# Kernel tuning notes

Hardware: AMD Instinct MI355X
Metric: run time of the kernel (lower is better)

## Reference

```python
import jax, jax.numpy as jnp
import numpy as np

DIM = 512
HEADS = 8
DIM_HEAD = 64
INNER = HEADS * DIM_HEAD  # 512
TOPK_FRAC = 0.7
SCALE = DIM_HEAD ** -0.5


def setup_inputs() -> dict:
    key = jax.random.key(0)
    k1, k2, k3, k4 = jax.random.split(key, 4)
    B, N = 4, 1024
    x = jax.random.normal(k1, (B, N, DIM), dtype=jnp.float32)
    # nn.Linear(dim, inner*3, bias=False): weight [3*inner, dim]; store transposed for x @ W
    w_qkv = jax.random.normal(k2, (DIM, 3 * INNER), dtype=jnp.float32) * (DIM ** -0.5)
    # to_out Linear(inner, dim) with bias
    w_out = jax.random.normal(k3, (INNER, DIM), dtype=jnp.float32) * (INNER ** -0.5)
    b_out = jax.random.normal(k4, (DIM,), dtype=jnp.float32) * 0.01
    return {"x": x, "w_qkv": w_qkv, "w_out": w_out, "b_out": b_out}


def reference(x, w_qkv, w_out, b_out):
    B, N, _ = x.shape
    H, D = HEADS, DIM_HEAD
    qkv = x @ w_qkv  # [B, N, 3*INNER]
    q, k, v = jnp.split(qkv, 3, axis=-1)
    # 'b n (h d) -> b h n d'
    reshape = lambda t: t.reshape(B, N, H, D).transpose(0, 2, 1, 3)
    q, k, v = reshape(q), reshape(k), reshape(v)
    dots = jnp.einsum('bhid,bhjd->bhij', q, k) * SCALE  # [B, H, N, N]
    # per-row top-k masking (kNN attention)
    kk = int(N * TOPK_FRAC)
    _, idx = jax.lax.top_k(dots, kk)  # [B, H, N, kk]
    bi = jnp.arange(B)[:, None, None, None]
    hi = jnp.arange(H)[None, :, None, None]
    ii = jnp.arange(N)[None, None, :, None]
    mask = jnp.zeros_like(dots).at[bi, hi, ii, idx].set(1.0)
    dots = jnp.where(mask > 0, dots, jnp.float32(-jnp.inf))
    attn = jax.nn.softmax(dots, axis=-1)
    out = jnp.einsum('bhij,bhjd->bhid', attn, v)  # [B, H, N, D]
    out = out.transpose(0, 2, 1, 3).reshape(B, N, H * D)  # 'b h n d -> b n (h d)'
    return out @ w_out + b_out
```

## Files before the change

kernel.cpp:

```cpp
#include <hip/hip_runtime.h>
#include <cstddef>

#define B_      4
#define N_      1024
#define DIM_    512
#define H_      8
#define D_      64
#define INNER_  512
#define TRIPLE_ 1536
#define KK_     716
#define SCALE_  0.125f

typedef short bf16x8 __attribute__((ext_vector_type(8)));
typedef float f32x4  __attribute__((ext_vector_type(4)));
typedef unsigned short ushort_t;
typedef ushort_t us8 __attribute__((ext_vector_type(8)));

__device__ __forceinline__ unsigned short bf16_rne(float f) {
    unsigned u = __float_as_uint(f);
    return (unsigned short)((u + 0x7FFFu + ((u >> 16) & 1u)) >> 16);
}
__device__ __forceinline__ float bf16_f(unsigned short s) {
    return __uint_as_float((unsigned)s << 16);
}
__device__ __forceinline__ unsigned f2key(float f) {
    unsigned u = __float_as_uint(f);
    return u ^ ((u & 0x80000000u) ? 0xFFFFFFFFu : 0x80000000u);
}
__device__ __forceinline__ float key2f(unsigned k) {
    unsigned u = (k & 0x80000000u) ? (k ^ 0x80000000u) : ~k;
    return __uint_as_float(u);
}
__device__ __forceinline__ int wave_count(int lc) {
    int c = __popcll(__ballot(lc & 1));
    c += __popcll(__ballot(lc & 2)) << 1;
    c += __popcll(__ballot(lc & 4)) << 2;
    c += __popcll(__ballot(lc & 8)) << 3;
    c += __popcll(__ballot(lc & 16)) << 4;
    return c;
}
__device__ __forceinline__ int count_ge(const unsigned* key, unsigned kt) {
    int lc = 0;
#pragma unroll
    for (int m = 0; m < 16; ++m) lc += (key[m] >= kt) ? 1 : 0;
    return wave_count(lc);
}
__device__ __forceinline__ unsigned bisect_exact(const unsigned* key,
                                                 bool hlo, bool hhi,
                                                 float tlo, float thi) {
    unsigned klo = hlo ? f2key(tlo) : 0u;
    unsigned khi = hhi ? f2key(thi) : 0xFFFFFFFFu;
    while (khi - klo > 1u) {
        const unsigned km = klo + ((khi - klo) >> 1);
        const int c = count_ge(key, km);
        if (c >= KK_) { klo = km; if (c == KK_) break; }
        else khi = km;
    }
    return klo;
}
__device__ __forceinline__ void topk2(const unsigned* key0, const unsigned* key1,
                                      float mu0, float sg0, float mu1, float sg1,
                                      unsigned& out0, unsigned& out1) {
    bool done0 = false, done1 = false;
    float tlo0 = 0.f, thi0 = 0.f, tlo1 = 0.f, thi1 = 0.f;
    int   clo0 = 0,   chi0 = 0,   clo1 = 0,   chi1 = 0;
    bool  hlo0 = false, hhi0 = false, hlo1 = false, hhi1 = false;
    float t0 = mu0 - 0.52189f * sg0;
    float t1 = mu1 - 0.52189f * sg1;
    unsigned res0 = 0u, res1 = 0u;
    for (int it = 0; it < 10; ++it) {
        if (done0 & done1) break;
        const unsigned kt0 = f2key(t0);
        const unsigned kt1 = f2key(t1);
        int lc0 = 0, lc1 = 0;
#pragma unroll
        for (int m = 0; m < 16; ++m) {
            lc0 += (key0[m] >= kt0) ? 1 : 0;
            lc1 += (key1[m] >= kt1) ? 1 : 0;
        }
        const int c0 = wave_count(lc0);
        const int c1 = wave_count(lc1);
        if (!done0) {
            if (c0 == KK_) { res0 = kt0; done0 = true; }
            else {
                if (c0 > KK_) { tlo0 = t0; clo0 = c0; hlo0 = true; }
                else          { thi0 = t0; chi0 = c0; hhi0 = true; }
                float tn;
                if (hlo0 && hhi0) {
                    tn = tlo0 + (thi0 - tlo0) * ((float)(clo0 - KK_) / (float)(clo0 - chi0));
                } else {
                    const float z    = (t0 - mu0) / sg0;
                    const float dens = fmaxf(408.5f * __expf(-0.5f * z * z) / sg0, 1.f);
                    tn = t0 + (float)(c0 - KK_) / dens;
                }
                if (hlo0 && !(tn > tlo0)) tn = hhi0 ? 0.5f * (tlo0 + thi0) : tlo0 + 0.25f * sg0;
                if (hhi0 && !(tn < thi0)) tn = hlo0 ? 0.5f * (tlo0 + thi0) : thi0 - 0.25f * sg0;
                t0 = tn;
            }
        }
        if (!done1) {
            if (c1 == KK_) { res1 = kt1; done1 = true; }
            else {
                if (c1 > KK_) { tlo1 = t1; clo1 = c1; hlo1 = true; }
                else          { thi1 = t1; chi1 = c1; hhi1 = true; }
                float tn;
                if (hlo1 && hhi1) {
                    tn = tlo1 + (thi1 - tlo1) * ((float)(clo1 - KK_) / (float)(clo1 - chi1));
                } else {
                    const float z    = (t1 - mu1) / sg1;
                    const float dens = fmaxf(408.5f * __expf(-0.5f * z * z) / sg1, 1.f);
                    tn = t1 + (float)(c1 - KK_) / dens;
                }
                if (hlo1 && !(tn > tlo1)) tn = hhi1 ? 0.5f * (tlo1 + thi1) : tlo1 + 0.25f * sg1;
                if (hhi1 && !(tn < thi1)) tn = hlo1 ? 0.5f * (tlo1 + thi1) : thi1 - 0.25f * sg1;
                t1 = tn;
            }
        }
    }
    if (!done0) res0 = bisect_exact(key0, hlo0, hhi0, tlo0, thi0);
    if (!done1) res1 = bisect_exact(key1, hlo1, hhi1, tlo1, thi1);
    out0 = res0;
    out1 = res1;
}
__device__ __forceinline__ void split8(const float* __restrict__ src,
                                       bf16x8& h8, bf16x8& l8) {
    float4 a = *(const float4*)src;
    float4 b = *(const float4*)(src + 4);
    float v[8] = {a.x, a.y, a.z, a.w, b.x, b.y, b.z, b.w};
#pragma unroll
    for (int i = 0; i < 8; ++i) {
        ushort_t hb = bf16_rne(v[i]);
        h8[i] = (short)hb;
        l8[i] = (short)bf16_rne(v[i] - bf16_f(hb));
    }
}

__global__ __launch_bounds__(256) void conv_wT2(const float* __restrict__ Wq,
                                                const float* __restrict__ Wo,
                                                ushort_t* __restrict__ WqTh,
                                                ushort_t* __restrict__ WqTl,
                                                ushort_t* __restrict__ WoTh,
                                                ushort_t* __restrict__ WoTl) {
    __shared__ float tile[32][33];
    const bool isQ = blockIdx.x < 48;
    const int  nb  = (isQ ? blockIdx.x : blockIdx.x - 48) * 32;
    const int  kb  = blockIdx.y * 32;
    const int  Nn  = isQ ? TRIPLE_ : DIM_;
    const float* W = isQ ? Wq : Wo;
    ushort_t* Th   = isQ ? WqTh : WoTh;
    ushort_t* Tl   = isQ ? WqTl : WoTl;
    const int tx = threadIdx.x & 31, ty = threadIdx.x >> 5;
    for (int yy = ty; yy < 32; yy += 8)
        tile[yy][tx] = W[(size_t)(kb + yy) * Nn + nb + tx];
    __syncthreads();
    for (int yy = ty; yy < 32; yy += 8) {
        float v = tile[tx][yy];
        ushort_t hb = bf16_rne(v);
        size_t idx = (size_t)(nb + yy) * DIM_ + kb + tx;
        Th[idx] = hb;
        Tl[idx] = bf16_rne(v - bf16_f(hb));
    }
}

__global__ __launch_bounds__(256) void gemm_qkv_mfma(
    const float* __restrict__ X,
    const ushort_t* __restrict__ Wh, const ushort_t* __restrict__ Wl,
    ushort_t* __restrict__ Qh, ushort_t* __restrict__ Ql,
    ushort_t* __restrict__ Kh, ushort_t* __restrict__ Kl,
    ushort_t* __restrict__ Vt) {
    __shared__ ushort_t stile[4][4608];
    __shared__ ushort_t BshH[2][2048];
    __shared__ ushort_t BshL[2][2048];
    const int t = threadIdx.x, w = t >> 6, l = t & 63;
    const int ln = l & 15, quad = l >> 4;
    const int n0 = blockIdx.y * 64;
    const int m0 = blockIdx.x * 128 + w * 32;
    f32x4 acc[2][4] = {};
    {
        const size_t xrow0 = (size_t)(m0 + ln) * DIM_;
        const size_t xrow1 = (size_t)(m0 + 16 + ln) * DIM_;
        const int srow = t >> 2;
        const int sk   = (t & 3) << 3;
        const size_t gb = (size_t)(n0 + srow) * DIM_ + sk;
        us8 nh = *(const us8*)&Wh[gb];
        us8 nl = *(const us8*)&Wl[gb];
        *(us8*)&BshH[0][t * 8] = nh;
        *(us8*)&BshL[0][t * 8] = nl;
        int cur = 0;
        for (int k0 = 0; k0 < DIM_; k0 += 32) {
            const bool more = (k0 + 32) < DIM_;
            const size_t gnext = gb + (size_t)(more ? k0 + 32 : 0);
            nh = *(const us8*)&Wh[gnext];
            nl = *(const us8*)&Wl[gnext];
            __syncthreads();
            const int ko = k0 + quad * 8;
            bf16x8 ah0, al0, ah1, al1;
            split8(&X[xrow0 + ko], ah0, al0);
            split8(&X[xrow1 + ko], ah1, al1);
#pragma unroll
            for (int j = 0; j < 4; ++j) {
                const int slot = (((j << 4) + ln) << 5) + (quad << 3);
                bf16x8 bh = *(const bf16x8*)&BshH[cur][slot];
                bf16x8 bl = *(const bf16x8*)&BshL[cur][slot];
                acc[0][j] = __builtin_amdgcn_mfma_f32_16x16x32_bf16(ah0, bh, acc[0][j], 0, 0, 0);
                acc[0][j] = __builtin_amdgcn_mfma_f32_16x16x32_bf16(al0, bh, acc[0][j], 0, 0, 0);
                acc[0][j] = __builtin_amdgcn_mfma_f32_16x16x32_bf16(ah0, bl, acc[0][j], 0, 0, 0);
                acc[1][j] = __builtin_amdgcn_mfma_f32_16x16x32_bf16(ah1, bh, acc[1][j], 0, 0, 0);
                acc[1][j] = __builtin_amdgcn_mfma_f32_16x16x32_bf16(al1, bh, acc[1][j], 0, 0, 0);
                acc[1][j] = __builtin_amdgcn_mfma_f32_16x16x32_bf16(ah1, bl, acc[1][j], 0, 0, 0);
            }
            if (more) {
                *(us8*)&BshH[cur ^ 1][t * 8] = nh;
                *(us8*)&BshL[cur ^ 1][t * 8] = nl;
            }
            cur ^= 1;
        }
    }
    const int sec = n0 >> 9;
    const int h   = (n0 >> 6) & 7;
    ushort_t* tw  = stile[w];
    const int b = m0 >> 10, nnb = m0 & 1023;
    if (sec < 2) {
        ushort_t* Hp = sec ? Kh : Qh;
        ushort_t* Lp = sec ? Kl : Ql;
        const float qsc = sec ? 1.0f : SCALE_;
#pragma unroll
        for (int i = 0; i < 2; ++i)
#pragma unroll
            for (int j = 0; j < 4; ++j)
#pragma unroll
                for (int g = 0; g < 4; ++g) {
                    const float v = acc[i][j][g] * qsc;
                    const ushort_t hb = bf16_rne(v);
                    const ushort_t lb = bf16_rne(v - bf16_f(hb));
                    const int tok = i * 16 + quad * 4 + g;
                    const int d   = j * 16 + ln;
                    tw[tok * 72 + d]        = hb;
                    tw[2304 + tok * 72 + d] = lb;
                }
        __syncthreads();
        const size_t rowbase = ((size_t)(b * 8 + h) * 1024 + nnb) * 64;
        const int dd = (l & 7) * 8;
#pragma unroll
        for (int s = 0; s < 4; ++s) {
            const int tl = s * 8 + (l >> 3);
            const size_t off = rowbase + (size_t)tl * 64 + dd;
            *(us8*)&Hp[off] = *(const us8*)&tw[tl * 72 + dd];
            *(us8*)&Lp[off] = *(const us8*)&tw[2304 + tl * 72 + dd];
        }
    } else {
#pragma unroll
        for (int i = 0; i < 2; ++i)
#pragma unroll
            for (int j = 0; j < 4; ++j)
#pragma unroll
                for (int g = 0; g < 4; ++g)
                    tw[(j * 16 + ln) * 40 + i * 16 + quad * 4 + g] = bf16_rne(acc[i][j][g]);
        __syncthreads();
        const size_t vbase = (size_t)(b * 8 + h) * 65536 + nnb;
#pragma unroll
        for (int p = 0; p < 2; ++p) {
            const int d = (p << 5) + (l >> 1);
            const int c = (l & 1) << 4;
            ushort_t* dst = &Vt[vbase + (size_t)d * 1024 + c];
            *(us8*)dst       = *(const us8*)&tw[d * 40 + c];
            *(us8*)(dst + 8) = *(const us8*)&tw[d * 40 + c + 8];
        }
    }
}

__global__ __launch_bounds__(256) void gemm_out_mfma(
    const ushort_t* __restrict__ Ah, const ushort_t* __restrict__ Al,
    const ushort_t* __restrict__ Wh, const ushort_t* __restrict__ Wl,
    const float* __restrict__ bias, float* __restrict__ C) {
    __shared__ ushort_t BshH[2][2048];
    __shared__ ushort_t BshL[2][2048];
    const int t = threadIdx.x, w = t >> 6, l = t & 63;
    const int ln = l & 15, quad = l >> 4;
    const int n0 = blockIdx.y * 64;
    const int m0 = blockIdx.x * 128 + w * 32;
    f32x4 acc[2][4] = {};
    {
        const size_t arow0 = (size_t)(m0 + ln) * INNER_;
        const size_t arow1 = (size_t)(m0 + 16 + ln) * INNER_;
        const int srow = t >> 2;
        const int sk   = (t & 3) << 3;
        const size_t gb = (size_t)(n0 + srow) * INNER_ + sk;
        us8 nh = *(const us8*)&Wh[gb];
        us8 nl = *(const us8*)&Wl[gb];
        *(us8*)&BshH[0][t * 8] = nh;
        *(us8*)&BshL[0][t * 8] = nl;
        int cur = 0;
        for (int k0 = 0; k0 < INNER_; k0 += 32) {
            const bool more = (k0 + 32) < INNER_;
            const size_t gnext = gb + (size_t)(more ? k0 + 32 : 0);
            nh = *(const us8*)&Wh[gnext];
            nl = *(const us8*)&Wl[gnext];
            __syncthreads();
            const int ko = k0 + quad * 8;
            bf16x8 ah0 = *(const bf16x8*)&Ah[arow0 + ko];
            bf16x8 al0 = *(const bf16x8*)&Al[arow0 + ko];
            bf16x8 ah1 = *(const bf16x8*)&Ah[arow1 + ko];
            bf16x8 al1 = *(const bf16x8*)&Al[arow1 + ko];
#pragma unroll
            for (int j = 0; j < 4; ++j) {
                const int slot = (((j << 4) + ln) << 5) + (quad << 3);
                bf16x8 bh = *(const bf16x8*)&BshH[cur][slot];
                bf16x8 bl = *(const bf16x8*)&BshL[cur][slot];
                acc[0][j] = __builtin_amdgcn_mfma_f32_16x16x32_bf16(ah0, bh, acc[0][j], 0, 0, 0);
                acc[0][j] = __builtin_amdgcn_mfma_f32_16x16x32_bf16(al0, bh, acc[0][j], 0, 0, 0);
                acc[0][j] = __builtin_amdgcn_mfma_f32_16x16x32_bf16(ah0, bl, acc[0][j], 0, 0, 0);
                acc[1][j] = __builtin_amdgcn_mfma_f32_16x16x32_bf16(ah1, bh, acc[1][j], 0, 0, 0);
                acc[1][j] = __builtin_amdgcn_mfma_f32_16x16x32_bf16(al1, bh, acc[1][j], 0, 0, 0);
                acc[1][j] = __builtin_amdgcn_mfma_f32_16x16x32_bf16(ah1, bl, acc[1][j], 0, 0, 0);
            }
            if (more) {
                *(us8*)&BshH[cur ^ 1][t * 8] = nh;
                *(us8*)&BshL[cur ^ 1][t * 8] = nl;
            }
            cur ^= 1;
        }
    }
#pragma unroll
    for (int i = 0; i < 2; ++i)
#pragma unroll
        for (int j = 0; j < 4; ++j) {
            const int col = n0 + j * 16 + ln;
            const float bb = bias[col];
#pragma unroll
            for (int g = 0; g < 4; ++g) {
                const int token = m0 + i * 16 + quad * 4 + g;
                C[(size_t)token * DIM_ + col] = acc[i][j][g] + bb;
            }
        }
}

__global__ __launch_bounds__(512, 4) void attn_mfma(const ushort_t* __restrict__ Qh,
                                                    const ushort_t* __restrict__ Ql,
                                                    const ushort_t* __restrict__ Kh,
                                                    const ushort_t* __restrict__ Kl,
                                                    const ushort_t* __restrict__ Vt,
                                                    ushort_t* __restrict__ Oh,
                                                    ushort_t* __restrict__ Ol) {
    __shared__ float sdots[16 * 512];
    __shared__ float spartial[4][16][17];

    const int t    = threadIdx.x;
    const int w    = t >> 6;
    const int l    = t & 63;
    const int ln   = l & 15;
    const int quad = l >> 4;
    const int wg   = blockIdx.x;
    const int bh   = wg & 31;
    const int i0   = (wg >> 5) << 4;

    const size_t bhoff = (size_t)bh << 16;

    const ushort_t* qp  = Qh + bhoff + (size_t)(i0 + ln) * 64 + (quad << 3);
    const ushort_t* qlp = Ql + bhoff + (size_t)(i0 + ln) * 64 + (quad << 3);
    bf16x8 qh0 = *(const bf16x8*)qp;
    bf16x8 qh1 = *(const bf16x8*)(qp + 32);
    bf16x8 ql0 = *(const bf16x8*)qlp;
    bf16x8 ql1 = *(const bf16x8*)(qlp + 32);

    const int r0 = w << 1, r1 = r0 | 1;
    const int swz0 = (r0 & 7) << 2, swz1 = (r1 & 7) << 2;
    const float* s0 = &sdots[r0 << 9];
    const float* s1 = &sdots[r1 << 9];

    unsigned key0[16], key1[16];
    float sa0 = 0.f, sb0 = 0.f, sa1 = 0.f, sb1 = 0.f;

#pragma unroll
    for (int tt = 0; tt < 4; ++tt) {
        const int j0 = (w << 6) + (tt << 4);
        const ushort_t* kp  = Kh + bhoff + (size_t)(j0 + ln) * 64 + (quad << 3);
        const ushort_t* klp = Kl + bhoff + (size_t)(j0 + ln) * 64 + (quad << 3);
        bf16x8 kh0 = *(const bf16x8*)kp;
        bf16x8 kh1 = *(const bf16x8*)(kp + 32);
        bf16x8 kl0 = *(const bf16x8*)klp;
        bf16x8 kl1 = *(const bf16x8*)(klp + 32);
        f32x4 acc = {0.f, 0.f, 0.f, 0.f};
        acc = __builtin_amdgcn_mfma_f32_16x16x32_bf16(qh0, kh0, acc, 0, 0, 0);
        acc = __builtin_amdgcn_mfma_f32_16x16x32_bf16(qh1, kh1, acc, 0, 0, 0);
        acc = __builtin_amdgcn_mfma_f32_16x16x32_bf16(qh0, kl0, acc, 0, 0, 0);
        acc = __builtin_amdgcn_mfma_f32_16x16x32_bf16(qh1, kl1, acc, 0, 0, 0);
        acc = __builtin_amdgcn_mfma_f32_16x16x32_bf16(ql0, kh0, acc, 0, 0, 0);
        acc = __builtin_amdgcn_mfma_f32_16x16x32_bf16(ql1, kh1, acc, 0, 0, 0);
#pragma unroll
        for (int g = 0; g < 4; ++g) {
            const int row = (quad << 2) + g;
            sdots[(row << 9) + ((j0 + ln) ^ ((row & 7) << 2))] = acc[g];
        }
    }
    __syncthreads();
#pragma unroll
    for (int m = 0; m < 2; ++m) {
        f32x4 kv0 = *(const f32x4*)&s0[((l << 2) + (m << 8)) ^ swz0];
        f32x4 kv1 = *(const f32x4*)&s1[((l << 2) + (m << 8)) ^ swz1];
#pragma unroll
        for (int i = 0; i < 4; ++i) {
            key0[(m << 2) + i] = f2key(kv0[i]);
            key1[(m << 2) + i] = f2key(kv1[i]);
            sa0 += kv0[i];
            sb0 += kv0[i] * kv0[i];
            sa1 += kv1[i];
            sb1 += kv1[i] * kv1[i];
        }
    }
    __syncthreads();

#pragma unroll
    for (int tt = 0; tt < 4; ++tt) {
        const int j0 = 512 + (w << 6) + (tt << 4);
        const ushort_t* kp  = Kh + bhoff + (size_t)(j0 + ln) * 64 + (quad << 3);
        const ushort_t* klp = Kl + bhoff + (size_t)(j0 + ln) * 64 + (quad << 3);
        bf16x8 kh0 = *(const bf16x8*)kp;
        bf16x8 kh1 = *(const bf16x8*)(kp + 32);
        bf16x8 kl0 = *(const bf16x8*)klp;
        bf16x8 kl1 = *(const bf16x8*)(klp + 32);
        f32x4 acc = {0.f, 0.f, 0.f, 0.f};
        acc = __builtin_amdgcn_mfma_f32_16x16x32_bf16(qh0, kh0, acc, 0, 0, 0);
        acc = __builtin_amdgcn_mfma_f32_16x16x32_bf16(qh1, kh1, acc, 0, 0, 0);
        acc = __builtin_amdgcn_mfma_f32_16x16x32_bf16(qh0, kl0, acc, 0, 0, 0);
        acc = __builtin_amdgcn_mfma_f32_16x16x32_bf16(qh1, kl1, acc, 0, 0, 0);
        acc = __builtin_amdgcn_mfma_f32_16x16x32_bf16(ql0, kh0, acc, 0, 0, 0);
        acc = __builtin_amdgcn_mfma_f32_16x16x32_bf16(ql1, kh1, acc, 0, 0, 0);
#pragma unroll
        for (int g = 0; g < 4; ++g) {
            const int row = (quad << 2) + g;
            const int jl  = (j0 - 512) + ln;
            sdots[(row << 9) + (jl ^ ((row & 7) << 2))] = acc[g];
        }
    }
    __syncthreads();
#pragma unroll
    for (int m = 0; m < 2; ++m) {
        f32x4 kv0 = *(const f32x4*)&s0[((l << 2) + (m << 8)) ^ swz0];
        f32x4 kv1 = *(const f32x4*)&s1[((l << 2) + (m << 8)) ^ swz1];
#pragma unroll
        for (int i = 0; i < 4; ++i) {
            key0[8 + (m << 2) + i] = f2key(kv0[i]);
            key1[8 + (m << 2) + i] = f2key(kv1[i]);
            sa0 += kv0[i];
            sb0 += kv0[i] * kv0[i];
            sa1 += kv1[i];
            sb1 += kv1[i] * kv1[i];
        }
    }

    ushort_t* sP = (ushort_t*)sdots;
    {
#pragma unroll
        for (int off = 32; off; off >>= 1) {
            sa0 += __shfl_xor(sa0, off, 64);
            sb0 += __shfl_xor(sb0, off, 64);
            sa1 += __shfl_xor(sa1, off, 64);
            sb1 += __shfl_xor(sb1, off, 64);
        }
        const float mu0 = sa0 * (1.0f / 1024.f);
        const float sg0 = sqrtf(fmaxf(sb0 * (1.0f / 1024.f) - mu0 * mu0, 1e-20f));
        const float mu1 = sa1 * (1.0f / 1024.f);
        const float sg1 = sqrtf(fmaxf(sb1 * (1.0f / 1024.f) - mu1 * mu1, 1e-20f));

        unsigned res0, res1;
        topk2(key0, key1, mu0, sg0, mu1, sg1, res0, res1);

        const float thr0 = key2f(res0), thr1 = key2f(res1);
        float pv0[16], pv1[16];
        float ls0 = 0.f, ls1 = 0.f;
#pragma unroll
        for (int m = 0; m < 16; ++m) {
            float p0 = (key0[m] >= res0) ? __expf(key2f(key0[m]) - thr0) : 0.f;
            float p1 = (key1[m] >= res1) ? __expf(key2f(key1[m]) - thr1) : 0.f;
            pv0[m] = p0;
            pv1[m] = p1;
            ls0 += p0;
            ls1 += p1;
        }
#pragma unroll
        for (int off = 32; off; off >>= 1) {
            ls0 += __shfl_xor(ls0, off, 64);
            ls1 += __shfl_xor(ls1, off, 64);
        }
        const float inv0 = 1.f / ls0, inv1 = 1.f / ls1;
#pragma unroll
        for (int m = 0; m < 4; ++m) {
            const int g0 = ((l >> 1) + (m << 5)) ^ (r0 & 7);
            const int g1 = ((l >> 1) + (m << 5)) ^ (r1 & 7);
            ushort4 pk0 = make_ushort4(bf16_rne(pv0[(m << 2) + 0] * inv0),
                                       bf16_rne(pv0[(m << 2) + 1] * inv0),
                                       bf16_rne(pv0[(m << 2) + 2] * inv0),
                                       bf16_rne(pv0[(m << 2) + 3] * inv0));
            ushort4 pk1 = make_ushort4(bf16_rne(pv1[(m << 2) + 0] * inv1),
                                       bf16_rne(pv1[(m << 2) + 1] * inv1),
                                       bf16_rne(pv1[(m << 2) + 2] * inv1),
                                       bf16_rne(pv1[(m << 2) + 3] * inv1));
            *(ushort4*)&sP[(r0 << 10) + (g0 << 3) + ((l & 1) << 2)] = pk0;
            *(ushort4*)&sP[(r1 << 10) + (g1 << 3) + ((l & 1) << 2)] = pk1;
        }
    }
    __syncthreads();

    const int dblk  = w & 3;
    const int jbase = (w & 4) << 7;
    f32x4 oacc = {0.f, 0.f, 0.f, 0.f};
    const ushort_t* vp =
        Vt + bhoff + (size_t)((dblk << 4) + ln) * 1024 + (quad << 3) + jbase;
    const int prow = ln << 10;
    const int rsw  = ln & 7;
#pragma unroll
    for (int j0 = 0; j0 < 512; j0 += 32) {
        const int g = ((jbase + j0) >> 3) + quad;
        bf16x8 af = *(const bf16x8*)&sP[prow + ((g ^ rsw) << 3)];
        bf16x8 bv = *(const bf16x8*)(vp + j0);
        oacc = __builtin_amdgcn_mfma_f32_16x16x32_bf16(af, bv, oacc, 0, 0, 0);
    }
    if (w & 4) {
#pragma unroll
        for (int g = 0; g < 4; ++g)
            spartial[dblk][(quad << 2) + g][ln] = oacc[g];
    }
    __syncthreads();
    if (!(w & 4)) {
        const int b = bh >> 3, h = bh & 7;
        const size_t obase =
            ((size_t)(b << 10) + i0 + (quad << 2)) * 512 + (h << 6) + (dblk << 4) + ln;
#pragma unroll
        for (int g = 0; g < 4; ++g) {
            const float v = oacc[g] + spartial[dblk][(quad << 2) + g][ln];
            ushort_t hb = bf16_rne(v);
            Oh[obase + (size_t)g * 512] = hb;
            Ol[obase + (size_t)g * 512] = bf16_rne(v - bf16_f(hb));
        }
    }
}

extern "C" void kernel_launch(void* const* d_in, const int* in_sizes, int n_in,
                              void* d_out, int out_size, void* d_ws, size_t ws_size,
                              hipStream_t stream) {
    const float* x     = (const float*)d_in[0];
    const float* w_qkv = (const float*)d_in[1];
    const float* w_out = (const float*)d_in[2];
    const float* b_out = (const float*)d_in[3];
    float*       out   = (float*)d_out;

    const size_t ON  = (size_t)4096 * 512;
    const size_t WQT = (size_t)1536 * 512;
    const size_t WOT = (size_t)512 * 512;
    const size_t QK  = (size_t)32 * 1024 * 64;

    ushort_t* p    = (ushort_t*)d_ws;
    ushort_t* Oh   = p;            p += ON;
    ushort_t* Ol   = p;            p += ON;
    ushort_t* WqTh = p;            p += WQT;
    ushort_t* WqTl = p;            p += WQT;
    ushort_t* WoTh = p;            p += WOT;
    ushort_t* WoTl = p;            p += WOT;
    ushort_t* Qh   = p;            p += QK;
    ushort_t* Ql   = p;            p += QK;
    ushort_t* Kh   = p;            p += QK;
    ushort_t* Kl   = p;            p += QK;
    ushort_t* Vt   = p;            p += QK;

    conv_wT2<<<dim3(64, 16), 256, 0, stream>>>(w_qkv, w_out, WqTh, WqTl, WoTh, WoTl);

    gemm_qkv_mfma<<<dim3(4096 / 128, TRIPLE_ / 64), 256, 0, stream>>>(
        x, WqTh, WqTl, Qh, Ql, Kh, Kl, Vt);

    attn_mfma<<<dim3(B_ * H_ * (N_ / 16)), 512, 0, stream>>>(Qh, Ql, Kh, Kl, Vt, Oh, Ol);

    gemm_out_mfma<<<dim3(4096 / 128, DIM_ / 64), 256, 0, stream>>>(
        Oh, Ol, WoTh, WoTl, b_out, out);
}
```

Before: 231.1 us.

## Compute full QK row in one pass, prefetch V and split MFMA accumulators

After: 222.3 us. 3.8% less time.

```diff
diff --git a/kernel.cpp b/kernel.cpp
--- a/kernel.cpp
+++ b/kernel.cpp
@@ -342,7 +342,7 @@
                                                     const ushort_t* __restrict__ Vt,
                                                     ushort_t* __restrict__ Oh,
                                                     ushort_t* __restrict__ Ol) {
-    __shared__ float sdots[16 * 512];
+    __shared__ float sdots[16 * 1024];
     __shared__ float spartial[4][16][17];
 
     const int t    = threadIdx.x;
@@ -363,17 +363,14 @@
     bf16x8 ql0 = *(const bf16x8*)qlp;
     bf16x8 ql1 = *(const bf16x8*)(qlp + 32);
 
-    const int r0 = w << 1, r1 = r0 | 1;
-    const int swz0 = (r0 & 7) << 2, swz1 = (r1 & 7) << 2;
-    const float* s0 = &sdots[r0 << 9];
-    const float* s1 = &sdots[r1 << 9];
-
-    unsigned key0[16], key1[16];
-    float sa0 = 0.f, sb0 = 0.f, sa1 = 0.f, sb1 = 0.f;
-
-#pragma unroll
-    for (int tt = 0; tt < 4; ++tt) {
-        const int j0 = (w << 6) + (tt << 4);
+    const int dblk  = w & 3;
+    const int jbase = (w & 4) << 7;
+    const ushort_t* vp =
+        Vt + bhoff + (size_t)((dblk << 4) + ln) * 1024 + (quad << 3) + jbase;
+    bf16x8 vpre[8];
+
+    for (int tt = 0; tt < 8; ++tt) {
+        const int j0 = ((w << 3) + tt) << 4;
         const ushort_t* kp  = Kh + bhoff + (size_t)(j0 + ln) * 64 + (quad << 3);
         const ushort_t* klp = Kl + bhoff + (size_t)(j0 + ln) * 64 + (quad << 3);
         bf16x8 kh0 = *(const bf16x8*)kp;
@@ -390,67 +387,33 @@
 #pragma unroll
         for (int g = 0; g < 4; ++g) {
             const int row = (quad << 2) + g;
-            sdots[(row << 9) + ((j0 + ln) ^ ((row & 7) << 2))] = acc[g];
+            sdots[(row << 10) + ((j0 + ln) ^ ((row & 7) << 2))] = acc[g];
         }
     }
     __syncthreads();
-#pragma unroll
-    for (int m = 0; m < 2; ++m) {
-        f32x4 kv0 = *(const f32x4*)&s0[((l << 2) + (m << 8)) ^ swz0];
-        f32x4 kv1 = *(const f32x4*)&s1[((l << 2) + (m << 8)) ^ swz1];
-#pragma unroll
-        for (int i = 0; i < 4; ++i) {
-            key0[(m << 2) + i] = f2key(kv0[i]);
-            key1[(m << 2) + i] = f2key(kv1[i]);
-            sa0 += kv0[i];
-            sb0 += kv0[i] * kv0[i];
-            sa1 += kv1[i];
-            sb1 += kv1[i] * kv1[i];
-        }
-    }
-    __syncthreads();
-
-#pragma unroll
-    for (int tt = 0; tt < 4; ++tt) {
-        const int j0 = 512 + (w << 6) + (tt << 4);
-        const ushort_t* kp  = Kh + bhoff + (size_t)(j0 + ln) * 64 + (quad << 3);
-        const ushort_t* klp = Kl + bhoff + (size_t)(j0 + ln) * 64 + (quad << 3);
-        bf16x8 kh0 = *(const bf16x8*)kp;
-        bf16x8 kh1 = *(const bf16x8*)(kp + 32);
-        bf16x8 kl0 = *(const bf16x8*)klp;
-        bf16x8 kl1 = *(const bf16x8*)(klp + 32);
-        f32x4 acc = {0.f, 0.f, 0.f, 0.f};
-        acc = __builtin_amdgcn_mfma_f32_16x16x32_bf16(qh0, kh0, acc, 0, 0, 0);
-        acc = __builtin_amdgcn_mfma_f32_16x16x32_bf16(qh1, kh1, acc, 0, 0, 0);
-        acc = __builtin_amdgcn_mfma_f32_16x16x32_bf16(qh0, kl0, acc, 0, 0, 0);
-        acc = __builtin_amdgcn_mfma_f32_16x16x32_bf16(qh1, kl1, acc, 0, 0, 0);
-        acc = __builtin_amdgcn_mfma_f32_16x16x32_bf16(ql0, kh0, acc, 0, 0, 0);
-        acc = __builtin_amdgcn_mfma_f32_16x16x32_bf16(ql1, kh1, acc, 0, 0, 0);
-#pragma unroll
-        for (int g = 0; g < 4; ++g) {
-            const int row = (quad << 2) + g;
-            const int jl  = (j0 - 512) + ln;
-            sdots[(row << 9) + (jl ^ ((row & 7) << 2))] = acc[g];
-        }
-    }
-    __syncthreads();
-#pragma unroll
-    for (int m = 0; m < 2; ++m) {
-        f32x4 kv0 = *(const f32x4*)&s0[((l << 2) + (m << 8)) ^ swz0];
-        f32x4 kv1 = *(const f32x4*)&s1[((l << 2) + (m << 8)) ^ swz1];
-#pragma unroll
-        for (int i = 0; i < 4; ++i) {
-            key0[8 + (m << 2) + i] = f2key(kv0[i]);
-            key1[8 + (m << 2) + i] = f2key(kv1[i]);
-            sa0 += kv0[i];
-            sb0 += kv0[i] * kv0[i];
-            sa1 += kv1[i];
-            sb1 += kv1[i] * kv1[i];
-        }
-    }
 
     ushort_t* sP = (ushort_t*)sdots;
     {
+        const int r0 = w << 1, r1 = r0 | 1;
+        const int swz0 = (r0 & 7) << 2, swz1 = (r1 & 7) << 2;
+        const float* s0 = &sdots[r0 << 10];
+        const float* s1 = &sdots[r1 << 10];
+        unsigned key0[16], key1[16];
+        float sa0 = 0.f, sb0 = 0.f, sa1 = 0.f, sb1 = 0.f;
+#pragma unroll
+        for (int m = 0; m < 4; ++m) {
+            f32x4 kv0 = *(const f32x4*)&s0[((l << 2) + (m << 8)) ^ swz0];
+            f32x4 kv1 = *(const f32x4*)&s1[((l << 2) + (m << 8)) ^ swz1];
+#pragma unroll
+            for (int i = 0; i < 4; ++i) {
+                key0[(m << 2) + i] = f2key(kv0[i]);
+                key1[(m << 2) + i] = f2key(kv1[i]);
+                sa0 += kv0[i];
+                sb0 += kv0[i] * kv0[i];
+                sa1 += kv1[i];
+                sb1 += kv1[i] * kv1[i];
+            }
+        }
 #pragma unroll
         for (int off = 32; off; off >>= 1) {
             sa0 += __shfl_xor(sa0, off, 64);
@@ -478,6 +441,9 @@
             ls0 += p0;
             ls1 += p1;
         }
+#pragma unroll
+        for (int p = 0; p < 8; ++p)
+            vpre[p] = *(const bf16x8*)(vp + p * 32);
 #pragma unroll
         for (int off = 32; off; off >>= 1) {
             ls0 += __shfl_xor(ls0, off, 64);
@@ -496,26 +462,37 @@
                                        bf16_rne(pv1[(m << 2) + 1] * inv1),
                                        bf16_rne(pv1[(m << 2) + 2] * inv1),
                                        bf16_rne(pv1[(m << 2) + 3] * inv1));
-            *(ushort4*)&sP[(r0 << 10) + (g0 << 3) + ((l & 1) << 2)] = pk0;
-            *(ushort4*)&sP[(r1 << 10) + (g1 << 3) + ((l & 1) << 2)] = pk1;
+            *(ushort4*)&sP[(r0 << 11) + (g0 << 3) + ((l & 1) << 2)] = pk0;
+            *(ushort4*)&sP[(r1 << 11) + (g1 << 3) + ((l & 1) << 2)] = pk1;
         }
     }
     __syncthreads();
 
-    const int dblk  = w & 3;
-    const int jbase = (w & 4) << 7;
-    f32x4 oacc = {0.f, 0.f, 0.f, 0.f};
-    const ushort_t* vp =
-        Vt + bhoff + (size_t)((dblk << 4) + ln) * 1024 + (quad << 3) + jbase;
-    const int prow = ln << 10;
+    const int prow = ln << 11;
     const int rsw  = ln & 7;
-#pragma unroll
-    for (int j0 = 0; j0 < 512; j0 += 32) {
+    bf16x8 vnx[8];
+#pragma unroll
+    for (int p = 0; p < 8; ++p)
+        vnx[p] = *(const bf16x8*)(vp + 256 + p * 32);
+    f32x4 oa[4] = {};
+    __builtin_amdgcn_s_setprio(1);
+#pragma unroll
+    for (int p = 0; p < 8; ++p) {
+        const int j0 = p * 32;
         const int g = ((jbase + j0) >> 3) + quad;
         bf16x8 af = *(const bf16x8*)&sP[prow + ((g ^ rsw) << 3)];
-        bf16x8 bv = *(const bf16x8*)(vp + j0);
-        oacc = __builtin_amdgcn_mfma_f32_16x16x32_bf16(af, bv, oacc, 0, 0, 0);
-    }
+        oa[p & 3] = __builtin_amdgcn_mfma_f32_16x16x32_bf16(af, vpre[p], oa[p & 3], 0, 0, 0);
+    }
+#pragma unroll
+    for (int p = 0; p < 8; ++p) {
+        const int j0 = 256 + p * 32;
+        const int g = ((jbase + j0) >> 3) + quad;
+        bf16x8 af = *(const bf16x8*)&sP[prow + ((g ^ rsw) << 3)];
+        oa[p & 3] = __builtin_amdgcn_mfma_f32_16x16x32_bf16(af, vnx[p], oa[p & 3], 0, 0, 0);
+    }
+    __builtin_amdgcn_s_setprio(0);
+    f32x4 oacc = (oa[0] + oa[1]) + (oa[2] + oa[3]);
+
     if (w & 4) {
 #pragma unroll
         for (int g = 0; g < 4; ++g)
```
